# Kernel optimization log

Measured on AMD Instinct MI355X. Metric: run time of the kernel, lower is better.

Reference implementation:

```python
import jax, jax.numpy as jnp
import numpy as np

N_NODES = 50000
N_EDGES = 1000000
HIDDEN = 64
NUM_GRAPHS = 512
EPS = 1e-5


def _instance_norm(x, seg, num_graphs):
    # per-graph, per-channel normalization (PyG InstanceNorm, affine=False)
    ones = jnp.ones((x.shape[0], 1), x.dtype)
    cnt = jnp.clip(jax.ops.segment_sum(ones, seg, num_segments=num_graphs), 1.0)
    mean = jax.ops.segment_sum(x, seg, num_segments=num_graphs) / cnt
    xc = x - mean[seg]
    var = jax.ops.segment_sum(xc * xc, seg, num_segments=num_graphs) / cnt
    return xc * jax.lax.rsqrt(var + EPS)[seg]


def setup_inputs() -> dict:
    key = jax.random.key(0)
    ks = jax.random.split(key, 10)
    emb = jax.random.normal(ks[0], (N_NODES, HIDDEN), jnp.float32)
    edge_index = jax.random.randint(ks[1], (2, N_EDGES), 0, N_NODES, jnp.int64 if jax.config.read('jax_enable_x64') else jnp.int32)
    batch = jnp.sort(jax.random.randint(ks[2], (N_NODES,), 0, NUM_GRAPHS))
    h = HIDDEN
    # channels = [2h, 4h, h, 1]
    W1 = jax.random.normal(ks[3], (2 * h, 4 * h), jnp.float32) * 0.05
    b1 = jnp.zeros((4 * h,), jnp.float32)
    W2 = jax.random.normal(ks[4], (4 * h, h), jnp.float32) * 0.05
    b2 = jnp.zeros((h,), jnp.float32)
    W3 = jax.random.normal(ks[5], (h, 1), jnp.float32) * 0.05
    b3 = jnp.zeros((1,), jnp.float32)
    return {"emb": emb, "W1": W1, "b1": b1, "W2": W2, "b2": b2,
            "W3": W3, "b3": b3, "edge_index": edge_index, "batch": batch}


def reference(emb, W1, b1, W2, b2, W3, b3, edge_index, batch):
    col, row = edge_index[0], edge_index[1]
    f12 = jnp.concatenate([emb[col], emb[row]], axis=-1)  # [E, 2h]
    seg = batch[col]  # per-edge graph id
    x = f12 @ W1 + b1                                      # [E, 4h]
    x = jax.nn.relu(_instance_norm(x, seg, NUM_GRAPHS))
    x = x @ W2 + b2                                        # [E, h]
    x = jax.nn.relu(_instance_norm(x, seg, NUM_GRAPHS))
    return x @ W3 + b3                                     # [E, 1]
```

## Files before the change

### kernel.cpp

```cpp
#include <hip/hip_runtime.h>
#include <hip/hip_bf16.h>

#define EDGES 1000000
#define NNODES 50000
#define NG 512
#define NTILES 15625
#define NCOLB 50176

typedef __attribute__((ext_vector_type(8))) short bf16x8;
typedef __attribute__((ext_vector_type(4))) float f32x4;

__device__ __forceinline__ unsigned short f2bf(float f){
  unsigned u = __float_as_uint(f);
  u += 0x7fffu + ((u >> 16) & 1u);
  return (unsigned short)(u >> 16);
}
__device__ __forceinline__ float bf2f(unsigned short h){
  return __uint_as_float(((unsigned)h) << 16);
}
__device__ __forceinline__ unsigned pk2bf(float x, float y){
  __hip_bfloat162 h = __float22bfloat162_rn(make_float2(x, y));
  union { __hip_bfloat162 h; unsigned u; } cv; cv.h = h;
  return cv.u;
}
__device__ __forceinline__ int xcd_swizzle(int bid, int nb){
  int nb8 = nb & ~7;
  if (bid >= nb8) return bid;
  int per = nb8 >> 3;
  return (bid & 7) * per + (bid >> 3);
}

__global__ void prep_all(const float* __restrict__ emb, const float* __restrict__ W1,
                         const float* __restrict__ W2,
                         unsigned short* __restrict__ emb_bf,
                         unsigned short* __restrict__ w1tn, unsigned short* __restrict__ w2t){
  int i = blockIdx.x * 256 + threadIdx.x;
  if (i < NNODES * 64){
    emb_bf[i] = f2bf(emb[i]);
  } else {
    int j = i - NNODES * 64;
    if (j < 32768){
      int jj = j >> 6, k = j & 63;
      float v = (jj < 256) ? W1[k * 256 + jj] : W1[(k + 64) * 256 + (jj - 256)];
      w1tn[j] = f2bf(v);
    } else {
      int jj = j - 32768;
      if (jj < 16384){
        int n = jj >> 8, k = jj & 255;
        w2t[jj] = f2bf(W2[k * 64 + n]);
      }
    }
  }
}

__global__ void hists(const int* __restrict__ ei, const int* __restrict__ batch,
                      unsigned* __restrict__ hist, unsigned* __restrict__ chist){
  __shared__ unsigned h[NG];
  int t = threadIdx.x;
  h[t] = 0; h[t + 256] = 0;
  __syncthreads();
  for (int i = 0; i < 4; i++){
    int e = blockIdx.x * 1024 + i * 256 + t;
    if (e < EDGES){
      int cn = ei[e];
      atomicAdd(&chist[cn], 1u);
      atomicAdd(&h[batch[cn]], 1u);
    }
  }
  __syncthreads();
  atomicAdd(&hist[t], h[t]);
  atomicAdd(&hist[t + 256], h[t + 256]);
}

__global__ void col_scan1(const unsigned* __restrict__ chist, unsigned* __restrict__ cpre,
                          unsigned* __restrict__ bsum){
  __shared__ unsigned s[256];
  int t = threadIdx.x;
  int i = blockIdx.x * 256 + t;
  unsigned v = (i < NNODES) ? chist[i] : 0u;
  s[t] = v;
  __syncthreads();
  for (int o = 1; o < 256; o <<= 1){
    unsigned u = (t >= o) ? s[t - o] : 0u;
    __syncthreads();
    s[t] += u;
    __syncthreads();
  }
  cpre[i] = s[t] - v;
  if (t == 255) bsum[blockIdx.x] = s[255];
}

__global__ void col_scan2(unsigned* __restrict__ bsum){
  __shared__ unsigned s[256];
  int t = threadIdx.x;
  unsigned v = (t < 196) ? bsum[t] : 0u;
  s[t] = v;
  __syncthreads();
  for (int o = 1; o < 256; o <<= 1){
    unsigned u = (t >= o) ? s[t - o] : 0u;
    __syncthreads();
    s[t] += u;
    __syncthreads();
  }
  if (t < 196) bsum[t] = s[t] - v;
}

__global__ void col_scan3(unsigned* __restrict__ cpre, const unsigned* __restrict__ bsum){
  int i = blockIdx.x * 256 + threadIdx.x;
  cpre[i] += bsum[blockIdx.x];
}

__global__ void col_scatter(const int* __restrict__ ei, const int* __restrict__ batch,
                            unsigned* __restrict__ cpre, int4* __restrict__ emeta){
  for (int i = 0; i < 4; i++){
    int e = blockIdx.x * 1024 + i * 256 + threadIdx.x;
    if (e < EDGES){
      int cn = ei[e];
      int pos = (int)atomicAdd(&cpre[cn], 1u);
      emeta[pos] = make_int4(cn, ei[EDGES + e], batch[cn], e);
    }
  }
}

__global__ __launch_bounds__(256) void node_gemm(
    const unsigned short* __restrict__ emb_bf, const unsigned short* __restrict__ w1tn,
    unsigned short* __restrict__ P)
{
  __shared__ unsigned short As[64 * 72];
  int t = threadIdx.x;
  int n0 = blockIdx.x * 64;
  {
    int nl = t >> 2, part = t & 3;
    int node = n0 + nl; if (node >= NNODES) node = 0;
    const int4* src = (const int4*)(emb_bf + node * 64 + part * 16);
    int4* dst = (int4*)(As + nl * 72 + part * 16);
    dst[0] = src[0]; dst[1] = src[1];
  }
  __syncthreads();
  int w = t >> 6, lane = t & 63, q = lane >> 4, c = lane & 15;
  f32x4 acc[4][8];
  for (int a = 0; a < 4; a++) for (int b = 0; b < 8; b++) for (int r = 0; r < 4; r++) acc[a][b][r] = 0.f;
  for (int k0 = 0; k0 < 64; k0 += 32){
    bf16x8 af[4];
    for (int tt = 0; tt < 4; tt++) af[tt] = *(const bf16x8*)(As + (tt * 16 + c) * 72 + k0 + q * 8);
    for (int n4 = 0; n4 < 8; n4++){
      bf16x8 bw = *(const bf16x8*)(w1tn + (w * 128 + n4 * 16 + c) * 64 + k0 + q * 8);
      for (int tt = 0; tt < 4; tt++)
        acc[tt][n4] = __builtin_amdgcn_mfma_f32_16x16x32_bf16(af[tt], bw, acc[tt][n4], 0, 0, 0);
    }
  }
  for (int tt = 0; tt < 4; tt++){
    for (int r = 0; r < 4; r++){
      int node = n0 + tt * 16 + q * 4 + r;
      if (node < NNODES){
        unsigned short* dst = P + (size_t)node * 512 + w * 128 + c;
        for (int n4 = 0; n4 < 8; n4++) dst[n4 * 16] = f2bf(acc[tt][n4][r]);
      }
    }
  }
}

__global__ __launch_bounds__(256, 5) void k1_gather(
    const unsigned short* __restrict__ P, const int4* __restrict__ emeta,
    float* __restrict__ sum1, float* __restrict__ sqs1)
{
  __shared__ float ls[1024];
  int t = threadIdx.x;
  int bid = xcd_swizzle(blockIdx.x, gridDim.x);
  int tile0 = bid * 8;
  for (int i = t; i < 1024; i += 256) ls[i] = 0.f;
  int s0 = emeta[tile0 * 64].z;
  int elast = tile0 * 64 + 511; if (elast >= EDGES) elast = EDGES - 1;
  int s1 = emeta[elast].z;
  __syncthreads();

  int w = t >> 6, lane = t & 63, c4 = lane * 4;

  float sm0 = 0.f, sm1 = 0.f, sm2 = 0.f, sm3 = 0.f;
  float q0 = 0.f, q1 = 0.f, q2 = 0.f, q3 = 0.f;
  int curs = -1;

  auto FLUSH = [&](int s){
    if (s == s0 || s == s1){
      float* base = ls + ((s == s0) ? 0 : 512) + c4;
      atomicAdd(base + 0, sm0); atomicAdd(base + 1, sm1);
      atomicAdd(base + 2, sm2); atomicAdd(base + 3, sm3);
      atomicAdd(base + 256, q0); atomicAdd(base + 257, q1);
      atomicAdd(base + 258, q2); atomicAdd(base + 259, q3);
    } else {
      float* sp = sum1 + s * 256 + c4;
      float* qp = sqs1 + s * 256 + c4;
      atomicAdd(sp + 0, sm0); atomicAdd(sp + 1, sm1); atomicAdd(sp + 2, sm2); atomicAdd(sp + 3, sm3);
      atomicAdd(qp + 0, q0);  atomicAdd(qp + 1, q1);  atomicAdd(qp + 2, q2);  atomicAdd(qp + 3, q3);
    }
    sm0 = sm1 = sm2 = sm3 = 0.f; q0 = q1 = q2 = q3 = 0.f;
  };

  for (int ti = 0; ti < 2; ti++){
    int tile = tile0 + w * 2 + ti;
    if (tile >= NTILES) continue;
    int4 me = emeta[tile * 64 + lane];
    int sseg = __builtin_amdgcn_readlane(me.z, 0);
    bool uni = (__ballot(me.z == sseg) == ~0ull);
    if (uni){
      if (sseg != curs){
        if (curs >= 0) FLUSH(curs);
        curs = sseg;
      }
      ushort4 rv[3][4], cv[3][4];
      #pragma unroll
      for (int g = 0; g < 2; g++){
        #pragma unroll
        for (int j = 0; j < 4; j++){
          int e = g * 4 + j;
          int re = __builtin_amdgcn_readlane(me.y, e);
          int ce = __builtin_amdgcn_readlane(me.x, e);
          rv[g][j] = *(const ushort4*)(P + (size_t)re * 512 + 256 + c4);
          cv[g][j] = *(const ushort4*)(P + (size_t)ce * 512 + c4);
        }
      }
      #pragma unroll
      for (int g = 0; g < 16; g++){
        if (g < 14){
          int bn = (g + 2) % 3;
          #pragma unroll
          for (int j = 0; j < 4; j++){
            int e = (g + 2) * 4 + j;
            int re = __builtin_amdgcn_readlane(me.y, e);
            int ce = __builtin_amdgcn_readlane(me.x, e);
            rv[bn][j] = *(const ushort4*)(P + (size_t)re * 512 + 256 + c4);
            cv[bn][j] = *(const ushort4*)(P + (size_t)ce * 512 + c4);
          }
        }
        int b = g % 3;
        #pragma unroll
        for (int j = 0; j < 4; j++){
          float x0 = bf2f(cv[b][j].x) + bf2f(rv[b][j].x);
          float x1 = bf2f(cv[b][j].y) + bf2f(rv[b][j].y);
          float x2v = bf2f(cv[b][j].z) + bf2f(rv[b][j].z);
          float x3 = bf2f(cv[b][j].w) + bf2f(rv[b][j].w);
          sm0 += x0; q0 += x0 * x0;
          sm1 += x1; q1 += x1 * x1;
          sm2 += x2v; q2 += x2v * x2v;
          sm3 += x3; q3 += x3 * x3;
        }
      }
    } else {
      int cprev = -1;
      ushort4 a = make_ushort4(0, 0, 0, 0);
      for (int e = 0; e < 64; e++){
        int ce = __builtin_amdgcn_readlane(me.x, e);
        int re = __builtin_amdgcn_readlane(me.y, e);
        int s = __builtin_amdgcn_readlane(me.z, e);
        if (s != curs){
          if (curs >= 0) FLUSH(curs);
          curs = s;
        }
        if (ce != cprev){ a = *(const ushort4*)(P + (size_t)ce * 512 + c4); cprev = ce; }
        ushort4 b = *(const ushort4*)(P + (size_t)re * 512 + 256 + c4);
        float x0 = bf2f(a.x) + bf2f(b.x);
        float x1 = bf2f(a.y) + bf2f(b.y);
        float x2v = bf2f(a.z) + bf2f(b.z);
        float x3 = bf2f(a.w) + bf2f(b.w);
        sm0 += x0; q0 += x0 * x0;
        sm1 += x1; q1 += x1 * x1;
        sm2 += x2v; q2 += x2v * x2v;
        sm3 += x3; q3 += x3 * x3;
      }
    }
  }
  if (curs >= 0) FLUSH(curs);

  __syncthreads();
  atomicAdd(&sum1[s0 * 256 + t], ls[t]);
  atomicAdd(&sqs1[s0 * 256 + t], ls[256 + t]);
  if (s1 != s0){
    atomicAdd(&sum1[s1 * 256 + t], ls[512 + t]);
    atomicAdd(&sqs1[s1 * 256 + t], ls[768 + t]);
  }
}

__global__ void finalize1(const float* __restrict__ sum1, const float* __restrict__ sqs1,
                          const unsigned* __restrict__ hist, float* __restrict__ r1,
                          float* __restrict__ mr1){
  int i = blockIdx.x * 256 + threadIdx.x;
  int g = i >> 8;
  float cnt = fmaxf((float)hist[g], 1.f);
  float m = sum1[i] / cnt;
  float v = sqs1[i] / cnt - m * m;
  v = fmaxf(v, 0.f);
  float r = rsqrtf(v + 1e-5f);
  r1[i] = r;
  mr1[i] = m * r;
}

__global__ void finalize2(const float* __restrict__ sum2, const float* __restrict__ sqs2,
                          const unsigned* __restrict__ hist, float* __restrict__ r2,
                          float* __restrict__ mr2){
  int i = blockIdx.x * 256 + threadIdx.x;
  int g = i >> 6;
  float cnt = fmaxf((float)hist[g], 1.f);
  float m = sum2[i] / cnt;
  float v = sqs2[i] / cnt - m * m;
  v = fmaxf(v, 0.f);
  float r = rsqrtf(v + 1e-5f);
  r2[i] = r;
  mr2[i] = m * r;
}

__global__ __launch_bounds__(256, 4) void k2_fused(
    const unsigned short* __restrict__ P, const unsigned short* __restrict__ w2t,
    const int4* __restrict__ emeta,
    const float* __restrict__ r1, const float* __restrict__ mr1,
    float* __restrict__ sum2, float* __restrict__ sqs2,
    unsigned short* __restrict__ x2t)
{
  __shared__ unsigned short Y[64 * 256];
  __shared__ int segl[64];
  __shared__ short rsegA[64];
  __shared__ unsigned char rloA[65];
  __shared__ int nrunS;
  int t = threadIdx.x;
  int bid = xcd_swizzle(blockIdx.x, gridDim.x);
  int p0 = bid * 64;
  int w = t >> 6, lane = t & 63, q = lane >> 4, c = lane & 15;
  int c4 = lane * 4;
  int elb0 = w * 16;
  int4 me = emeta[p0 + elb0 + (lane & 15)];

  ushort4 bb[16], cc[16];
  #pragma unroll
  for (int e = 0; e < 16; e++){
    int re = __builtin_amdgcn_readlane(me.y, e);
    int ce = __builtin_amdgcn_readlane(me.x, e);
    bb[e] = *(const ushort4*)(P + (size_t)re * 512 + 256 + c4);
    cc[e] = *(const ushort4*)(P + (size_t)ce * 512 + c4);
  }
  int s0g = __builtin_amdgcn_readlane(me.z, 0);
  float4 r4  = *(const float4*)(r1  + s0g * 256 + c4);
  float4 mr4 = *(const float4*)(mr1 + s0g * 256 + c4);

  if (t < 64) segl[t] = emeta[p0 + t].z;
  if (w == 0){
    int sN = segl[lane];
    int nxt = (lane < 63) ? segl[lane + 1] : sN;
    unsigned long long mask = __ballot(sN != nxt);
    if (lane == 0){
      if (mask == 0ull){
        nrunS = 1; rloA[0] = 0; rloA[1] = 64; rsegA[0] = (short)sN;
      } else {
        int n = 0, cur = segl[0];
        rsegA[0] = (short)cur; rloA[0] = 0;
        for (int i = 1; i < 64; i++)
          if (segl[i] != cur){ cur = segl[i]; n++; rsegA[n] = (short)cur; rloA[n] = (unsigned char)i; }
        rloA[n + 1] = 64; nrunS = n + 1;
      }
    }
  }
  __syncthreads();
  int nrun = nrunS;
  bool uni = (nrun == 1);

  #pragma unroll
  for (int e = 0; e < 16; e++){
    float4 rr4 = r4, mm4 = mr4;
    if (!uni){
      int s = __builtin_amdgcn_readlane(me.z, e);
      rr4 = *(const float4*)(r1  + s * 256 + c4);
      mm4 = *(const float4*)(mr1 + s * 256 + c4);
    }
    float y0 = fmaxf(0.f, (bf2f(cc[e].x) + bf2f(bb[e].x)) * rr4.x - mm4.x);
    float y1 = fmaxf(0.f, (bf2f(cc[e].y) + bf2f(bb[e].y)) * rr4.y - mm4.y);
    float y2 = fmaxf(0.f, (bf2f(cc[e].z) + bf2f(bb[e].z)) * rr4.z - mm4.z);
    float y3 = fmaxf(0.f, (bf2f(cc[e].w) + bf2f(bb[e].w)) * rr4.w - mm4.w);
    uint2 pk;
    pk.x = pk2bf(y0, y1);
    pk.y = pk2bf(y2, y3);
    int row = elb0 + e;
    *(uint2*)((char*)Y + row * 512 + ((lane * 8) ^ ((row & 7) << 4))) = pk;
  }
  __syncthreads();

  f32x4 acc2[4];
  for (int tt = 0; tt < 4; tt++) for (int r = 0; r < 4; r++) acc2[tt][r] = 0.f;
  int ch2 = w * 16 + c;
  int swzr = (c & 7) << 4;
  for (int kc = 0; kc < 8; kc++){
    bf16x8 bfr = *(const bf16x8*)(w2t + ch2 * 256 + kc * 32 + q * 8);
    int kb = (kc * 64 + q * 16) ^ swzr;
    for (int tt = 0; tt < 4; tt++){
      bf16x8 afr = *(const bf16x8*)((const char*)Y + (tt * 16 + c) * 512 + kb);
      acc2[tt] = __builtin_amdgcn_mfma_f32_16x16x32_bf16(afr, bfr, acc2[tt], 0, 0, 0);
    }
  }

  if (uni){
    int s = segl[0];
    float sm = 0.f, sq = 0.f;
    for (int tt = 0; tt < 4; tt++)
      for (int r = 0; r < 4; r++){
        float v = acc2[tt][r];
        sm += v; sq += v * v;
      }
    sm += __shfl_xor(sm, 16); sq += __shfl_xor(sq, 16);
    sm += __shfl_xor(sm, 32); sq += __shfl_xor(sq, 32);
    if (q == 0){
      atomicAdd(&sum2[s * 64 + ch2], sm);
      atomicAdd(&sqs2[s * 64 + ch2], sq);
    }
  } else {
    for (int rr = 0; rr < nrun; rr++){
      int s = rsegA[rr], lo = rloA[rr], hi = rloA[rr + 1];
      float sm = 0.f, sq = 0.f;
      for (int tt = 0; tt < 4; tt++){
        int elb = tt * 16 + q * 4;
        for (int r = 0; r < 4; r++){
          int el = elb + r;
          if (el >= lo && el < hi){
            float v = acc2[tt][r];
            sm += v; sq += v * v;
          }
        }
      }
      sm += __shfl_xor(sm, 16); sq += __shfl_xor(sq, 16);
      sm += __shfl_xor(sm, 32); sq += __shfl_xor(sq, 32);
      if (q == 0){
        atomicAdd(&sum2[s * 64 + ch2], sm);
        atomicAdd(&sqs2[s * 64 + ch2], sq);
      }
    }
  }
  for (int tt = 0; tt < 4; tt++){
    uint2 pk;
    pk.x = pk2bf(acc2[tt][0], acc2[tt][1]);
    pk.y = pk2bf(acc2[tt][2], acc2[tt][3]);
    *(uint2*)(x2t + (size_t)ch2 * EDGES + p0 + tt * 16 + q * 4) = pk;
  }
}

__global__ __launch_bounds__(256) void k3_out(
    const unsigned short* __restrict__ x2t, const int4* __restrict__ emeta,
    const float* __restrict__ r2, const float* __restrict__ mr2,
    const float* __restrict__ W3, const float* __restrict__ b3, float* __restrict__ out)
{
  int pp4 = (blockIdx.x * 256 + threadIdx.x) * 4;
  if (pp4 >= EDGES) return;
  int4 m0 = emeta[pp4 + 0];
  int4 m1 = emeta[pp4 + 1];
  int4 m2 = emeta[pp4 + 2];
  int4 m3 = emeta[pp4 + 3];
  float a0 = 0.f, a1 = 0.f, a2 = 0.f, a3 = 0.f;
  if (m0.z == m3.z && m0.z == m1.z && m0.z == m2.z){
    const float* rp = r2  + m0.z * 64;
    const float* mp = mr2 + m0.z * 64;
    #pragma unroll 8
    for (int ch = 0; ch < 64; ch++){
      ushort4 v = *(const ushort4*)(x2t + (size_t)ch * EDGES + pp4);
      float rr = rp[ch], mm = mp[ch], wv = W3[ch];
      a0 += fmaxf(0.f, bf2f(v.x) * rr - mm) * wv;
      a1 += fmaxf(0.f, bf2f(v.y) * rr - mm) * wv;
      a2 += fmaxf(0.f, bf2f(v.z) * rr - mm) * wv;
      a3 += fmaxf(0.f, bf2f(v.w) * rr - mm) * wv;
    }
  } else {
    #pragma unroll 8
    for (int ch = 0; ch < 64; ch++){
      ushort4 v = *(const ushort4*)(x2t + (size_t)ch * EDGES + pp4);
      float wv = W3[ch];
      a0 += fmaxf(0.f, bf2f(v.x) * r2[m0.z * 64 + ch] - mr2[m0.z * 64 + ch]) * wv;
      a1 += fmaxf(0.f, bf2f(v.y) * r2[m1.z * 64 + ch] - mr2[m1.z * 64 + ch]) * wv;
      a2 += fmaxf(0.f, bf2f(v.z) * r2[m2.z * 64 + ch] - mr2[m2.z * 64 + ch]) * wv;
      a3 += fmaxf(0.f, bf2f(v.w) * r2[m3.z * 64 + ch] - mr2[m3.z * 64 + ch]) * wv;
    }
  }
  float bv = b3[0];
  out[m0.w] = a0 + bv;
  out[m1.w] = a1 + bv;
  out[m2.w] = a2 + bv;
  out[m3.w] = a3 + bv;
}

extern "C" void kernel_launch(void* const* d_in, const int* in_sizes, int n_in,
                              void* d_out, int out_size, void* d_ws, size_t ws_size,
                              hipStream_t stream)
{
  (void)in_sizes; (void)n_in; (void)out_size;
  const float* emb = (const float*)d_in[0];
  const float* W1  = (const float*)d_in[1];
  const float* W2  = (const float*)d_in[3];
  const float* W3  = (const float*)d_in[5];
  const float* b3  = (const float*)d_in[6];
  const int* ei    = (const int*)d_in[7];
  const int* batch = (const int*)d_in[8];
  float* out = (float*)d_out;

  char* p = (char*)d_ws;
  size_t off = 0;
  auto take = [&](size_t n) -> char* {
    char* r = p + off;
    off += (n + 255) & ~(size_t)255;
    return r;
  };

  unsigned short* emb_bf = (unsigned short*)take((size_t)NNODES * 64 * 2);
  unsigned short* w1tn   = (unsigned short*)take(32768 * 2);
  unsigned short* w2t    = (unsigned short*)take(16384 * 2);
  int4* emeta = (int4*)take((size_t)EDGES * 16);
  unsigned short* P   = (unsigned short*)take((size_t)NNODES * 512 * 2);
  unsigned short* x2t = (unsigned short*)take((size_t)EDGES * 64 * 2);
  float* r1  = (float*)take(512 * 256 * 4);
  float* mr1 = (float*)take(512 * 256 * 4);
  float* r2  = (float*)take(512 * 64 * 4);
  float* mr2 = (float*)take(512 * 64 * 4);
  unsigned* cpre = (unsigned*)take(NCOLB * 4);
  unsigned* bsum = (unsigned*)take(256 * 4);
  char* zbase = p + off;
  unsigned* hist  = (unsigned*)take(NG * 4);
  unsigned* chist = (unsigned*)take(NCOLB * 4);
  float* sum1 = (float*)take(512 * 256 * 4);
  float* sqs1 = (float*)take(512 * 256 * 4);
  float* sum2 = (float*)take(512 * 64 * 4);
  float* sqs2 = (float*)take(512 * 64 * 4);
  size_t zsize = (size_t)((p + off) - zbase);

  if (ws_size < off) return;

  hipMemsetAsync(zbase, 0, zsize, stream);
  prep_all<<<12692, 256, 0, stream>>>(emb, W1, W2, emb_bf, w1tn, w2t);
  hists<<<977, 256, 0, stream>>>(ei, batch, hist, chist);
  col_scan1<<<196, 256, 0, stream>>>(chist, cpre, bsum);
  col_scan2<<<1, 256, 0, stream>>>(bsum);
  col_scan3<<<196, 256, 0, stream>>>(cpre, bsum);
  col_scatter<<<977, 256, 0, stream>>>(ei, batch, cpre, emeta);
  node_gemm<<<(NNODES + 63) / 64, 256, 0, stream>>>(emb_bf, w1tn, P);
  k1_gather<<<(NTILES + 7) / 8, 256, 0, stream>>>(P, emeta, sum1, sqs1);
  finalize1<<<512, 256, 0, stream>>>(sum1, sqs1, hist, r1, mr1);
  k2_fused<<<NTILES, 256, 0, stream>>>(P, w2t, emeta, r1, mr1, sum2, sqs2, x2t);
  finalize2<<<128, 256, 0, stream>>>(sum2, sqs2, hist, r2, mr2);
  k3_out<<<977, 256, 0, stream>>>(x2t, emeta, r2, mr2, W3, b3, out);
}
```

Baseline: 509.8 us.

## Gather row features straight into LDS and reuse repeated column loads

The per-edge row-node feature gather now uses global_load_lds, which writes directly into the shared Y tile, and is read back from LDS afterwards. The column-node gather keeps one register copy and only reloads when the column index changes between consecutive edges. This is meant to cut VGPR pressure and redundant gather traffic when edges are sorted by column. The cost is an extra LDS round trip. Correctness relies on the async load having completed before the block barrier.

```diff
diff --git a/kernel.cpp b/kernel.cpp
--- a/kernel.cpp
+++ b/kernel.cpp
@@ -22,6 +22,11 @@
   __hip_bfloat162 h = __float22bfloat162_rn(make_float2(x, y));
   union { __hip_bfloat162 h; unsigned u; } cv; cv.h = h;
   return cv.u;
+}
+__device__ __forceinline__ void gload_lds16(const void* g, void* l){
+  __builtin_amdgcn_global_load_lds(
+      (const __attribute__((address_space(1))) unsigned int*)g,
+      (__attribute__((address_space(3))) unsigned int*)l, 16, 0, 0);
 }
 __device__ __forceinline__ int xcd_swizzle(int bid, int nb){
   int nb8 = nb & ~7;
@@ -328,14 +333,17 @@
   int elb0 = w * 16;
   int4 me = emeta[p0 + elb0 + (lane & 15)];
 
-  ushort4 bb[16], cc[16];
   #pragma unroll
-  for (int e = 0; e < 16; e++){
-    int re = __builtin_amdgcn_readlane(me.y, e);
-    int ce = __builtin_amdgcn_readlane(me.x, e);
-    bb[e] = *(const ushort4*)(P + (size_t)re * 512 + 256 + c4);
-    cc[e] = *(const ushort4*)(P + (size_t)ce * 512 + c4);
-  }
+  for (int pp = 0; pp < 8; pp++){
+    int r0 = __builtin_amdgcn_readlane(me.y, 2 * pp);
+    int r1n = __builtin_amdgcn_readlane(me.y, 2 * pp + 1);
+    int node = (lane < 32) ? r0 : r1n;
+    const unsigned short* g = P + (size_t)node * 512 + 256 + (lane & 31) * 8;
+    gload_lds16(g, &Y[(elb0 + 2 * pp) * 256]);
+  }
+
+  int cprev = __builtin_amdgcn_readlane(me.x, 0);
+  ushort4 a = *(const ushort4*)(P + (size_t)cprev * 512 + c4);
   int s0g = __builtin_amdgcn_readlane(me.z, 0);
   float4 r4  = *(const float4*)(r1  + s0g * 256 + c4);
   float4 mr4 = *(const float4*)(mr1 + s0g * 256 + c4);
@@ -361,18 +369,25 @@
   int nrun = nrunS;
   bool uni = (nrun == 1);
 
+  ushort4 bb[16];
+  #pragma unroll
+  for (int e = 0; e < 16; e++)
+    bb[e] = *(const ushort4*)(Y + (elb0 + e) * 256 + c4);
+
   #pragma unroll
   for (int e = 0; e < 16; e++){
+    int ce = __builtin_amdgcn_readlane(me.x, e);
+    if (ce != cprev){ a = *(const ushort4*)(P + (size_t)ce * 512 + c4); cprev = ce; }
     float4 rr4 = r4, mm4 = mr4;
     if (!uni){
       int s = __builtin_amdgcn_readlane(me.z, e);
       rr4 = *(const float4*)(r1  + s * 256 + c4);
       mm4 = *(const float4*)(mr1 + s * 256 + c4);
     }
-    float y0 = fmaxf(0.f, (bf2f(cc[e].x) + bf2f(bb[e].x)) * rr4.x - mm4.x);
-    float y1 = fmaxf(0.f, (bf2f(cc[e].y) + bf2f(bb[e].y)) * rr4.y - mm4.y);
-    float y2 = fmaxf(0.f, (bf2f(cc[e].z) + bf2f(bb[e].z)) * rr4.z - mm4.z);
-    float y3 = fmaxf(0.f, (bf2f(cc[e].w) + bf2f(bb[e].w)) * rr4.w - mm4.w);
+    float y0 = fmaxf(0.f, (bf2f(a.x) + bf2f(bb[e].x)) * rr4.x - mm4.x);
+    float y1 = fmaxf(0.f, (bf2f(a.y) + bf2f(bb[e].y)) * rr4.y - mm4.y);
+    float y2 = fmaxf(0.f, (bf2f(a.z) + bf2f(bb[e].z)) * rr4.z - mm4.z);
+    float y3 = fmaxf(0.f, (bf2f(a.w) + bf2f(bb[e].w)) * rr4.w - mm4.w);
     uint2 pk;
     pk.x = pk2bf(y0, y1);
     pk.y = pk2bf(y2, y3);
```

Result: no change. 501.8 us (-1.6%).

## Build MFMA A-fragments directly in registers in k2, dropping LDS staging

Applied to the files above, without the earlier changes.

The second-layer kernel no longer stages normalized activations in shared memory. Each wave now owns 16 edges across all 64 output channels: every lane loads its own edge's col/row features and norm stats per k-chunk, builds the bf16 A fragment in registers, and issues 4 MFMAs against W2 fragments read from global memory. This removes LDS writes and reads, both __syncthreads barriers, and the serial single-lane segment-run scan, replacing the scan with a per-wave ballot. The trade is more global loads: W2 is loaded per wave rather than shared through LDS, r1/mr1 are loaded per edge, and feature gathers become 16-byte per-lane loads spread over scattered rows.

```diff
diff --git a/kernel.cpp b/kernel.cpp
--- a/kernel.cpp
+++ b/kernel.cpp
@@ -315,126 +315,103 @@
     float* __restrict__ sum2, float* __restrict__ sqs2,
     unsigned short* __restrict__ x2t)
 {
-  __shared__ unsigned short Y[64 * 256];
-  __shared__ int segl[64];
-  __shared__ short rsegA[64];
-  __shared__ unsigned char rloA[65];
-  __shared__ int nrunS;
   int t = threadIdx.x;
   int bid = xcd_swizzle(blockIdx.x, gridDim.x);
   int p0 = bid * 64;
   int w = t >> 6, lane = t & 63, q = lane >> 4, c = lane & 15;
-  int c4 = lane * 4;
-  int elb0 = w * 16;
-  int4 me = emeta[p0 + elb0 + (lane & 15)];
-
-  ushort4 bb[16], cc[16];
+  int e0 = w * 16;
+  int4 me = emeta[p0 + e0 + c];
+
+  const unsigned short* colp = P + (size_t)me.x * 512;
+  const unsigned short* rowp = P + (size_t)me.y * 512 + 256;
+  const float* rp = r1  + me.z * 256;
+  const float* mp = mr1 + me.z * 256;
+
+  f32x4 acc2[4];
   #pragma unroll
-  for (int e = 0; e < 16; e++){
-    int re = __builtin_amdgcn_readlane(me.y, e);
-    int ce = __builtin_amdgcn_readlane(me.x, e);
-    bb[e] = *(const ushort4*)(P + (size_t)re * 512 + 256 + c4);
-    cc[e] = *(const ushort4*)(P + (size_t)ce * 512 + c4);
-  }
-  int s0g = __builtin_amdgcn_readlane(me.z, 0);
-  float4 r4  = *(const float4*)(r1  + s0g * 256 + c4);
-  float4 mr4 = *(const float4*)(mr1 + s0g * 256 + c4);
-
-  if (t < 64) segl[t] = emeta[p0 + t].z;
-  if (w == 0){
-    int sN = segl[lane];
-    int nxt = (lane < 63) ? segl[lane + 1] : sN;
-    unsigned long long mask = __ballot(sN != nxt);
-    if (lane == 0){
-      if (mask == 0ull){
-        nrunS = 1; rloA[0] = 0; rloA[1] = 64; rsegA[0] = (short)sN;
-      } else {
-        int n = 0, cur = segl[0];
-        rsegA[0] = (short)cur; rloA[0] = 0;
-        for (int i = 1; i < 64; i++)
-          if (segl[i] != cur){ cur = segl[i]; n++; rsegA[n] = (short)cur; rloA[n] = (unsigned char)i; }
-        rloA[n + 1] = 64; nrunS = n + 1;
-      }
-    }
-  }
-  __syncthreads();
-  int nrun = nrunS;
-  bool uni = (nrun == 1);
+  for (int ng = 0; ng < 4; ng++)
+    #pragma unroll
+    for (int r = 0; r < 4; r++) acc2[ng][r] = 0.f;
 
   #pragma unroll
-  for (int e = 0; e < 16; e++){
-    float4 rr4 = r4, mm4 = mr4;
-    if (!uni){
-      int s = __builtin_amdgcn_readlane(me.z, e);
-      rr4 = *(const float4*)(r1  + s * 256 + c4);
-      mm4 = *(const float4*)(mr1 + s * 256 + c4);
-    }
-    float y0 = fmaxf(0.f, (bf2f(cc[e].x) + bf2f(bb[e].x)) * rr4.x - mm4.x);
-    float y1 = fmaxf(0.f, (bf2f(cc[e].y) + bf2f(bb[e].y)) * rr4.y - mm4.y);
-    float y2 = fmaxf(0.f, (bf2f(cc[e].z) + bf2f(bb[e].z)) * rr4.z - mm4.z);
-    float y3 = fmaxf(0.f, (bf2f(cc[e].w) + bf2f(bb[e].w)) * rr4.w - mm4.w);
-    uint2 pk;
-    pk.x = pk2bf(y0, y1);
-    pk.y = pk2bf(y2, y3);
-    int row = elb0 + e;
-    *(uint2*)((char*)Y + row * 512 + ((lane * 8) ^ ((row & 7) << 4))) = pk;
-  }
-  __syncthreads();
-
-  f32x4 acc2[4];
-  for (int tt = 0; tt < 4; tt++) for (int r = 0; r < 4; r++) acc2[tt][r] = 0.f;
-  int ch2 = w * 16 + c;
-  int swzr = (c & 7) << 4;
   for (int kc = 0; kc < 8; kc++){
-    bf16x8 bfr = *(const bf16x8*)(w2t + ch2 * 256 + kc * 32 + q * 8);
-    int kb = (kc * 64 + q * 16) ^ swzr;
-    for (int tt = 0; tt < 4; tt++){
-      bf16x8 afr = *(const bf16x8*)((const char*)Y + (tt * 16 + c) * 512 + kb);
-      acc2[tt] = __builtin_amdgcn_mfma_f32_16x16x32_bf16(afr, bfr, acc2[tt], 0, 0, 0);
-    }
-  }
-
+    int ch0 = kc * 32 + q * 8;
+    union { int4 i; unsigned short u[8]; } ua, ub;
+    ua.i = *(const int4*)(colp + ch0);
+    ub.i = *(const int4*)(rowp + ch0);
+    float4 rlo = *(const float4*)(rp + ch0);
+    float4 rhi = *(const float4*)(rp + ch0 + 4);
+    float4 mlo = *(const float4*)(mp + ch0);
+    float4 mhi = *(const float4*)(mp + ch0 + 4);
+    float y0 = fmaxf(0.f, (bf2f(ua.u[0]) + bf2f(ub.u[0])) * rlo.x - mlo.x);
+    float y1 = fmaxf(0.f, (bf2f(ua.u[1]) + bf2f(ub.u[1])) * rlo.y - mlo.y);
+    float y2 = fmaxf(0.f, (bf2f(ua.u[2]) + bf2f(ub.u[2])) * rlo.z - mlo.z);
+    float y3 = fmaxf(0.f, (bf2f(ua.u[3]) + bf2f(ub.u[3])) * rlo.w - mlo.w);
+    float y4 = fmaxf(0.f, (bf2f(ua.u[4]) + bf2f(ub.u[4])) * rhi.x - mhi.x);
+    float y5 = fmaxf(0.f, (bf2f(ua.u[5]) + bf2f(ub.u[5])) * rhi.y - mhi.y);
+    float y6 = fmaxf(0.f, (bf2f(ua.u[6]) + bf2f(ub.u[6])) * rhi.z - mhi.z);
+    float y7 = fmaxf(0.f, (bf2f(ua.u[7]) + bf2f(ub.u[7])) * rhi.w - mhi.w);
+    union { bf16x8 v; unsigned u[4]; } af;
+    af.u[0] = pk2bf(y0, y1);
+    af.u[1] = pk2bf(y2, y3);
+    af.u[2] = pk2bf(y4, y5);
+    af.u[3] = pk2bf(y6, y7);
+    #pragma unroll
+    for (int ng = 0; ng < 4; ng++){
+      bf16x8 bfr = *(const bf16x8*)(w2t + (ng * 16 + c) * 256 + ch0);
+      acc2[ng] = __builtin_amdgcn_mfma_f32_16x16x32_bf16(af.v, bfr, acc2[ng], 0, 0, 0);
+    }
+  }
+
+  int s0 = __builtin_amdgcn_readlane(me.z, 0);
+  bool uni = (__ballot(me.z == s0) == ~0ull);
   if (uni){
-    int s = segl[0];
-    float sm = 0.f, sq = 0.f;
-    for (int tt = 0; tt < 4; tt++)
-      for (int r = 0; r < 4; r++){
-        float v = acc2[tt][r];
-        sm += v; sq += v * v;
-      }
-    sm += __shfl_xor(sm, 16); sq += __shfl_xor(sq, 16);
-    sm += __shfl_xor(sm, 32); sq += __shfl_xor(sq, 32);
-    if (q == 0){
-      atomicAdd(&sum2[s * 64 + ch2], sm);
-      atomicAdd(&sqs2[s * 64 + ch2], sq);
-    }
-  } else {
-    for (int rr = 0; rr < nrun; rr++){
-      int s = rsegA[rr], lo = rloA[rr], hi = rloA[rr + 1];
-      float sm = 0.f, sq = 0.f;
-      for (int tt = 0; tt < 4; tt++){
-        int elb = tt * 16 + q * 4;
-        for (int r = 0; r < 4; r++){
-          int el = elb + r;
-          if (el >= lo && el < hi){
-            float v = acc2[tt][r];
-            sm += v; sq += v * v;
-          }
-        }
-      }
+    #pragma unroll
+    for (int ng = 0; ng < 4; ng++){
+      float sm = acc2[ng][0] + acc2[ng][1] + acc2[ng][2] + acc2[ng][3];
+      float sq = acc2[ng][0] * acc2[ng][0] + acc2[ng][1] * acc2[ng][1]
+               + acc2[ng][2] * acc2[ng][2] + acc2[ng][3] * acc2[ng][3];
       sm += __shfl_xor(sm, 16); sq += __shfl_xor(sq, 16);
       sm += __shfl_xor(sm, 32); sq += __shfl_xor(sq, 32);
       if (q == 0){
-        atomicAdd(&sum2[s * 64 + ch2], sm);
-        atomicAdd(&sqs2[s * 64 + ch2], sq);
-      }
-    }
-  }
-  for (int tt = 0; tt < 4; tt++){
+        atomicAdd(&sum2[s0 * 64 + ng * 16 + c], sm);
+        atomicAdd(&sqs2[s0 * 64 + ng * 16 + c], sq);
+      }
+    }
+  } else {
+    int prz = __shfl(me.z, (c == 0) ? 0 : (c - 1));
+    unsigned long long bm = __ballot((lane < 16) && (c > 0) && (me.z != prz));
+    int lo = 0;
+    while (true){
+      int hi = bm ? (int)__builtin_ctzll(bm) : 16;
+      int s = __builtin_amdgcn_readlane(me.z, lo);
+      #pragma unroll
+      for (int ng = 0; ng < 4; ng++){
+        float sm = 0.f, sq = 0.f;
+        #pragma unroll
+        for (int r = 0; r < 4; r++){
+          int el = q * 4 + r;
+          if (el >= lo && el < hi){ float v = acc2[ng][r]; sm += v; sq += v * v; }
+        }
+        sm += __shfl_xor(sm, 16); sq += __shfl_xor(sq, 16);
+        sm += __shfl_xor(sm, 32); sq += __shfl_xor(sq, 32);
+        if (q == 0){
+          atomicAdd(&sum2[s * 64 + ng * 16 + c], sm);
+          atomicAdd(&sqs2[s * 64 + ng * 16 + c], sq);
+        }
+      }
+      if (!bm) break;
+      lo = hi;
+      bm &= bm - 1;
+    }
+  }
+
+  #pragma unroll
+  for (int ng = 0; ng < 4; ng++){
     uint2 pk;
-    pk.x = pk2bf(acc2[tt][0], acc2[tt][1]);
-    pk.y = pk2bf(acc2[tt][2], acc2[tt][3]);
-    *(uint2*)(x2t + (size_t)ch2 * EDGES + p0 + tt * 16 + q * 4) = pk;
+    pk.x = pk2bf(acc2[ng][0], acc2[ng][1]);
+    pk.y = pk2bf(acc2[ng][2], acc2[ng][3]);
+    *(uint2*)(x2t + (size_t)(ng * 16 + c) * EDGES + p0 + e0 + q * 4) = pk;
   }
 }
 
```

Result: slower. 764.7 us (+50.0%).
